# Performance work log

Measured on AMD Instinct MI355X. Metric: run time of the kernel, lower is better.

Reference implementation:

```python
import math
import jax, jax.numpy as jnp
import numpy as np

T, B, C, H = 1024, 4, 1024, 16
D = C // H  # d_k = 64


def setup_inputs() -> dict:
    key = jax.random.key(0)
    ks = jax.random.split(key, 16)
    s = 0.02
    return {
        "query": jax.random.normal(ks[0], (T, B, C), jnp.float32),
        "key": jax.random.normal(ks[1], (T, B, C), jnp.float32),
        "value": jax.random.normal(ks[2], (T, B, C), jnp.float32),
        "pos_emb": jax.random.normal(ks[3], (2 * T - 1, 1, C), jnp.float32),
        "Wq": jax.random.normal(ks[4], (C, C), jnp.float32) * s,
        "bq": jnp.zeros((C,), jnp.float32),
        "Wk": jax.random.normal(ks[5], (C, C), jnp.float32) * s,
        "bk": jnp.zeros((C,), jnp.float32),
        "Wv": jax.random.normal(ks[6], (C, C), jnp.float32) * s,
        "bv": jnp.zeros((C,), jnp.float32),
        "Wp": jax.random.normal(ks[7], (C, C), jnp.float32) * s,
        "Wo": jax.random.normal(ks[8], (C, C), jnp.float32) * s,
        "bo": jnp.zeros((C,), jnp.float32),
        "pos_bias_u": jax.random.normal(ks[9], (H, D), jnp.float32) * s,
        "pos_bias_v": jax.random.normal(ks[10], (H, D), jnp.float32) * s,
    }


def rel_shift(x):
    # x: [B, H, T, P] with P = 2T-1 -> [B, H, T, T]
    b, h, t, p = x.shape
    x = jnp.pad(x, ((0, 0), (0, 0), (0, 0), (1, 0)))  # [B,H,T,P+1]
    x = x.reshape(b, h, p + 1, t)[:, :, 1:, :].reshape(b, h, t, p)
    return x[..., : p // 2 + 1]


def reference(query, key, value, pos_emb, Wq, bq, Wk, bk, Wv, bv, Wp, Wo, bo,
              pos_bias_u, pos_bias_v):
    # T x B x C -> B x T x C
    q_in = query.transpose(1, 0, 2)
    k_in = key.transpose(1, 0, 2)
    v_in = value.transpose(1, 0, 2)
    p_in = pos_emb.transpose(1, 0, 2)  # [1, 2T-1, C]

    q = (q_in @ Wq.T + bq).reshape(B, T, H, D)            # [B,T,H,D]
    k = (k_in @ Wk.T + bk).reshape(B, T, H, D)
    v = (v_in @ Wv.T + bv).reshape(B, T, H, D)
    p = (p_in @ Wp.T).reshape(2 * T - 1, H, D)            # [2T-1,H,D]

    # content (ac) and position (bd) scores
    matrix_ac = jnp.einsum('bthd,bshd->bhts', q + pos_bias_u, k)   # [B,H,T,T]
    matrix_bd = jnp.einsum('bthd,phd->bhtp', q + pos_bias_v, p)    # [B,H,T,2T-1]
    matrix_bd = rel_shift(matrix_bd)                               # [B,H,T,T]

    scores = (matrix_ac + matrix_bd) / math.sqrt(D)
    scores = jnp.clip(scores, -1e8, 1e8)
    attn = jax.nn.softmax(scores.astype(jnp.float32), axis=-1).astype(scores.dtype)

    x = jnp.einsum('bhts,bshd->bthd', attn, v).reshape(B, T, C)
    out = x @ Wo.T + bo
    return out.transpose(1, 0, 2)  # T x B x C
```

## Files before the change

kernel.cpp:

```cpp
#include <hip/hip_runtime.h>
#include <hip/hip_bf16.h>
#include <math.h>

#define T_SEQ 1024
#define NB 4
#define NH 16
#define DD 64
#define CC 1024

typedef __attribute__((ext_vector_type(8))) short short8;
typedef __attribute__((ext_vector_type(4))) float floatx4;
typedef __attribute__((ext_vector_type(4))) unsigned short ushort4v;

#define MFMA(a, b, c) __builtin_amdgcn_mfma_f32_16x16x32_bf16((a), (b), (c), 0, 0, 0)

__device__ inline float bf2f(unsigned short u) {
  union { unsigned int i; float f; } c; c.i = ((unsigned int)u) << 16; return c.f;
}
__device__ inline unsigned short f2bf(float x) {
  union { float f; unsigned int i; } c; c.f = x;
  unsigned int u = c.i;
  u += 0x7fff + ((u >> 16) & 1);
  return (unsigned short)(u >> 16);
}

__device__ __forceinline__ void gload_lds16(const void* g, void* l) {
  __builtin_amdgcn_global_load_lds(
      (const __attribute__((address_space(1))) unsigned int*)g,
      (__attribute__((address_space(3))) unsigned int*)l, 16, 0, 0);
}

__global__ __launch_bounds__(256) void convert_kernel(
    const float* __restrict__ q, const float* __restrict__ k,
    const float* __restrict__ v, const float* __restrict__ pe_in,
    const float* __restrict__ wq, const float* __restrict__ wk,
    const float* __restrict__ wv, const float* __restrict__ wp,
    const float* __restrict__ wo,
    unsigned short* __restrict__ qo, unsigned short* __restrict__ ko,
    unsigned short* __restrict__ vo, unsigned short* __restrict__ po,
    unsigned short* __restrict__ wqo, unsigned short* __restrict__ wko,
    unsigned short* __restrict__ wvo, unsigned short* __restrict__ wpo,
    unsigned short* __restrict__ woo)
{
  const int i = blockIdx.x * 256 + threadIdx.x;
  const float* src; unsigned short* dst; int off;
  if      (i < 524288)  { src = q;     dst = qo;  off = i; }
  else if (i < 1048576) { src = k;     dst = ko;  off = i - 524288; }
  else if (i < 1572864) { src = v;     dst = vo;  off = i - 1048576; }
  else if (i < 1834880) { src = pe_in; dst = po;  off = i - 1572864; }
  else if (i < 1965952) { src = wq;    dst = wqo; off = i - 1834880; }
  else if (i < 2097024) { src = wk;    dst = wko; off = i - 1965952; }
  else if (i < 2228096) { src = wv;    dst = wvo; off = i - 2097024; }
  else if (i < 2359168) { src = wp;    dst = wpo; off = i - 2228096; }
  else if (i < 2490240) { src = wo;    dst = woo; off = i - 2359168; }
  else {
    const int j = i - 2490240;
    *(short8*)&po[2047 * 1024 + j * 8] = (short8){0, 0, 0, 0, 0, 0, 0, 0};
    return;
  }
  const float4 a0 = *(const float4*)(src + (size_t)off * 8);
  const float4 a1 = *(const float4*)(src + (size_t)off * 8 + 4);
  short8 val = (short8){(short)f2bf(a0.x), (short)f2bf(a0.y), (short)f2bf(a0.z), (short)f2bf(a0.w),
                        (short)f2bf(a1.x), (short)f2bf(a1.y), (short)f2bf(a1.z), (short)f2bf(a1.w)};
  *(short8*)&dst[(size_t)off * 8] = val;
}

template <int OUT_BF16>
__device__ __forceinline__ void gemm_core(
    const unsigned short* __restrict__ A, const unsigned short* __restrict__ Wt,
    const float* __restrict__ bias, void* __restrict__ Cv,
    unsigned short* As, unsigned short* Bs, int N, int K, int bm, int bn)
{
  const int tid = threadIdx.x;
  const int lane = tid & 63;
  const int w = tid >> 6;
  const int l15 = lane & 15, quad = lane >> 4;
  const int rw = (w >> 1) * 64, cw = (w & 1) * 64;

  floatx4 acc[4][4];
#pragma unroll
  for (int i = 0; i < 4; ++i)
#pragma unroll
    for (int j = 0; j < 4; ++j) acc[i][j] = (floatx4){0.f, 0.f, 0.f, 0.f};

  const int lrow = lane >> 2, lcol = (lane & 3) * 8;
  const unsigned short* Ag = A + (size_t)(bm + w * 32 + lrow) * K + lcol;
  const unsigned short* Wg = Wt + (size_t)(bn + w * 32 + lrow) * K + lcol;
  unsigned short* AsW = As + w * 1024;
  unsigned short* BsW = Bs + w * 1024;

  for (int k0 = 0; k0 < K; k0 += 32) {
    gload_lds16(Ag + k0, AsW);
    gload_lds16(Ag + 16 * K + k0, AsW + 512);
    gload_lds16(Wg + k0, BsW);
    gload_lds16(Wg + 16 * K + k0, BsW + 512);
    __syncthreads();

    short8 af[4], bfr[4];
#pragma unroll
    for (int i = 0; i < 4; ++i)
      af[i] = *(short8*)&As[(rw + i * 16 + l15) * 32 + quad * 8];
#pragma unroll
    for (int j = 0; j < 4; ++j)
      bfr[j] = *(short8*)&Bs[(cw + j * 16 + l15) * 32 + quad * 8];
#pragma unroll
    for (int i = 0; i < 4; ++i)
#pragma unroll
      for (int j = 0; j < 4; ++j)
        acc[i][j] = MFMA(af[i], bfr[j], acc[i][j]);
    __syncthreads();
  }

#pragma unroll
  for (int j = 0; j < 4; ++j) {
    const int col = bn + cw + j * 16 + l15;
    const float bj = bias ? bias[col] : 0.f;
#pragma unroll
    for (int i = 0; i < 4; ++i) {
      const int row0 = bm + rw + i * 16 + quad * 4;
#pragma unroll
      for (int reg = 0; reg < 4; ++reg) {
        const float v = acc[i][j][reg] + bj;
        if (OUT_BF16)
          ((unsigned short*)Cv)[(size_t)(row0 + reg) * N + col] = f2bf(v);
        else
          ((float*)Cv)[(size_t)(row0 + reg) * N + col] = v;
      }
    }
  }
}

struct GemmJob { const unsigned short* A; const unsigned short* Wt;
                 const float* bias; unsigned short* C; int mtiles; };
struct GemmJobs { GemmJob j[4]; };

__global__ __launch_bounds__(256) void gemm_qkvp(GemmJobs jobs) {
  __shared__ __align__(16) unsigned short As[128 * 32];
  __shared__ __align__(16) unsigned short Bs[128 * 32];
  GemmJob jb = jobs.j[blockIdx.z];
  if ((int)blockIdx.y >= jb.mtiles) return;
  gemm_core<1>(jb.A, jb.Wt, jb.bias, jb.C, As, Bs, 1024, 1024,
               blockIdx.y * 128, blockIdx.x * 128);
}

template <int OUT_BF16>
__global__ __launch_bounds__(256) void gemm_one(
    const unsigned short* __restrict__ A, const unsigned short* __restrict__ Wt,
    const float* __restrict__ bias, void* __restrict__ Cv) {
  __shared__ __align__(16) unsigned short As[128 * 32];
  __shared__ __align__(16) unsigned short Bs[128 * 32];
  gemm_core<OUT_BF16>(A, Wt, bias, Cv, As, Bs, 1024, 1024,
                      blockIdx.y * 128, blockIdx.x * 128);
}

__global__ __launch_bounds__(256) void transpose_v(
    const unsigned short* __restrict__ vb, unsigned short* __restrict__ vT)
{
  __shared__ __align__(16) unsigned short Lt[64 * 136];
  const int t0 = blockIdx.x * 128;
  const int h = blockIdx.y, b = blockIdx.z;
  const int tid = threadIdx.x;

#pragma unroll
  for (int cc = 0; cc < 4; ++cc) {
    const int idx = tid + cc * 256;
    const int r = idx >> 3, pc = idx & 7;
    short8 val = *(const short8*)(vb + ((size_t)((t0 + r) * 4 + b)) * 1024 + h * 64 + pc * 8);
#pragma unroll
    for (int e = 0; e < 8; ++e)
      Lt[(pc * 8 + e) * 136 + r] = (unsigned short)val[e];
  }
  __syncthreads();
#pragma unroll
  for (int cc = 0; cc < 4; ++cc) {
    const int idx = tid + cc * 256;
    const int d = idx >> 4, tc = idx & 15;
    short8 v2 = *(short8*)&Lt[d * 136 + tc * 8];
    *(short8*)(vT + ((size_t)((b * 16 + h) * 64 + d)) * 1024 + t0 + tc * 8) = v2;
  }
}

__global__ __launch_bounds__(256) void precompute_kernel(
    const unsigned short* __restrict__ kb, const unsigned short* __restrict__ pb,
    const float* __restrict__ pbu, const float* __restrict__ pbv,
    float* __restrict__ uk, float* __restrict__ vp)
{
  const int i = blockIdx.x * 256 + threadIdx.x;
  if (i < 65536) {
    const int b = i >> 14, h = (i >> 10) & 15, s = i & 1023;
    const unsigned short* kr = kb + ((size_t)(s * 4 + b)) * 1024 + h * 64;
    const float* ur = pbu + h * 64;
    float sum = 0.f;
#pragma unroll
    for (int c = 0; c < 8; ++c) {
      short8 kv = *(const short8*)(kr + c * 8);
#pragma unroll
      for (int e = 0; e < 8; ++e) sum += bf2f((unsigned short)kv[e]) * ur[c * 8 + e];
    }
    uk[i] = sum;
  } else if (i < 98304) {
    const int j = i - 65536;
    const int idx = j >> 4, h = j & 15;
    const unsigned short* pr = pb + (size_t)idx * 1024 + h * 64;
    const float* vr = pbv + h * 64;
    float sum = 0.f;
#pragma unroll
    for (int c = 0; c < 8; ++c) {
      short8 pv = *(const short8*)(pr + c * 8);
#pragma unroll
      for (int e = 0; e < 8; ++e) sum += bf2f((unsigned short)pv[e]) * vr[c * 8 + e];
    }
    vp[(idx << 4) + h] = sum;
  }
}

#define BDW 148

__global__ __launch_bounds__(256) void attn_kernel(
    const unsigned short* __restrict__ qb, const unsigned short* __restrict__ kb,
    const unsigned short* __restrict__ pb, const unsigned short* __restrict__ vT,
    const float* __restrict__ uk, const float* __restrict__ vp,
    unsigned short* __restrict__ xb)
{
  __shared__ __align__(16) float SMEM_ALL[10240];
  float* BDf  = SMEM_ALL;
  unsigned short* Pb = (unsigned short*)SMEM_ALL;
  float* uk_s  = SMEM_ALL + 9472;
  float* vp_w  = SMEM_ALL + 9600;
  float* pmax0 = SMEM_ALL + 9792;
  float* pmax1 = SMEM_ALL + 9856;
  float* psum0 = SMEM_ALL + 9920;
  float* psum1 = SMEM_ALL + 9984;
  float* m_rowA = SMEM_ALL + 10048;
  float* m_rowB = SMEM_ALL + 10112;
  float* l_row  = SMEM_ALL + 10176;

  const int tid = threadIdx.x;
  const int lane = tid & 63;
  const int w = tid >> 6;
  const int l15 = lane & 15, quad = lane >> 4;
  const int th = w & 1, sh = w >> 1;

  const int flat = blockIdx.x + (blockIdx.y << 4) + (blockIdx.z << 8);
  const int x8 = flat & 7, s8 = flat >> 3;
  const int hb = x8 * 8 + (s8 >> 4);
  const int t0 = (s8 & 15) * 64;
  const int b = hb >> 4, h = hb & 15;

  short8 qf[2][2];
#pragma unroll
  for (int tt = 0; tt < 2; ++tt)
#pragma unroll
    for (int kk = 0; kk < 2; ++kk) {
      const int t = t0 + th * 32 + tt * 16 + l15;
      qf[tt][kk] = *(const short8*)(qb + ((size_t)(t * 4 + b)) * 1024 + h * 64 + kk * 32 + quad * 8);
    }

  floatx4 of[2][2];
#pragma unroll
  for (int i = 0; i < 2; ++i)
#pragma unroll
    for (int j = 0; j < 2; ++j) of[i][j] = (floatx4){0.f, 0.f, 0.f, 0.f};

  if (tid < 64) { m_rowA[tid] = -3.0e38f; l_row[tid] = 0.f; }
  __syncthreads();

  const unsigned short* kbase = kb + ((size_t)((sh * 64 + l15) * 4 + b)) * 1024 + h * 64;
  const unsigned short* pbase0 = pb + ((size_t)(sh * 96 + l15)) * 1024 + h * 64;

  short8 kf[4][2], pf[6][2];
  {
    const int w0 = 0 - t0 + 960;
#pragma unroll
    for (int st4 = 0; st4 < 4; ++st4) {
      const unsigned short* kr = kbase + (size_t)(st4 * 16) * 4096;
      kf[st4][0] = *(const short8*)(kr + quad * 8);
      kf[st4][1] = *(const short8*)(kr + 32 + quad * 8);
    }
#pragma unroll
    for (int jt = 0; jt < 6; ++jt) {
      const int sA = sh * 96 + jt * 16 + th * 32;
      if (sA <= 16 || sA > 190) continue;
      const unsigned short* pr = pbase0 + (size_t)(w0 + jt * 16) * 1024;
      pf[jt][0] = *(const short8*)(pr + quad * 8);
      pf[jt][1] = *(const short8*)(pr + 32 + quad * 8);
    }
  }

  for (int s0 = 0; s0 < 1024; s0 += 128) {
    const int w0 = s0 - t0 + 960;
    const int par = (s0 >> 7) & 1;
    float* m_prev = par ? m_rowB : m_rowA;
    float* m_next = par ? m_rowA : m_rowB;

    if (tid < 128) uk_s[tid] = uk[((b * 16 + h) << 10) + s0 + tid];
    if (tid < 192) vp_w[tid] = vp[(((size_t)(w0 + tid)) << 4) + h];

#pragma unroll
    for (int jt = 0; jt < 6; ++jt) {
      const int jjbase = sh * 96 + jt * 16;
#pragma unroll
      for (int tt = 0; tt < 2; ++tt) {
        const int tbase = th * 32 + tt * 16;
        const int ssum = jjbase + tbase;
        if (ssum <= 32 || ssum > 190) continue;
        floatx4 z = (floatx4){0.f, 0.f, 0.f, 0.f};
        z = MFMA(pf[jt][0], qf[tt][0], z);
        z = MFMA(pf[jt][1], qf[tt][1], z);
        const int tloc = tbase + l15;
        *(float4*)&BDf[tloc * BDW + (ssum - 48) + quad * 4] =
            make_float4(z[0], z[1], z[2], z[3]);
      }
    }

    floatx4 st[4][2];
#pragma unroll
    for (int stile = 0; stile < 4; ++stile) {
#pragma unroll
      for (int tt = 0; tt < 2; ++tt) {
        floatx4 z = (floatx4){0.f, 0.f, 0.f, 0.f};
        z = MFMA(kf[stile][0], qf[tt][0], z);
        z = MFMA(kf[stile][1], qf[tt][1], z);
        st[stile][tt] = z;
      }
    }

    {
      const int s0n = (s0 + 128 < 1024) ? (s0 + 128) : 0;
      const int w0n = s0n - t0 + 960;
#pragma unroll
      for (int st4 = 0; st4 < 4; ++st4) {
        const unsigned short* kr = kbase + (size_t)(s0n + st4 * 16) * 4096;
        kf[st4][0] = *(const short8*)(kr + quad * 8);
        kf[st4][1] = *(const short8*)(kr + 32 + quad * 8);
      }
#pragma unroll
      for (int jt = 0; jt < 6; ++jt) {
        const int sA = sh * 96 + jt * 16 + th * 32;
        if (sA <= 16 || sA > 190) continue;
        const unsigned short* pr = pbase0 + (size_t)(w0n + jt * 16) * 1024;
        pf[jt][0] = *(const short8*)(pr + quad * 8);
        pf[jt][1] = *(const short8*)(pr + 32 + quad * 8);
      }
    }
    __syncthreads();

    float lmax[2] = {-3.0e38f, -3.0e38f};
#pragma unroll
    for (int stile = 0; stile < 4; ++stile)
#pragma unroll
      for (int tt = 0; tt < 2; ++tt) {
        const int tloc = th * 32 + tt * 16 + l15;
#pragma unroll
        for (int reg = 0; reg < 4; ++reg) {
          const int sloc = sh * 64 + stile * 16 + quad * 4 + reg;
          const int jj = sloc - tloc + 63;
          float v = 0.125f * (st[stile][tt][reg] + BDf[tloc * BDW + sloc - l15 + 15] +
                              uk_s[sloc] + vp_w[jj]);
          st[stile][tt][reg] = v;
          lmax[tt] = fmaxf(lmax[tt], v);
        }
      }
#pragma unroll
    for (int tt = 0; tt < 2; ++tt) {
      lmax[tt] = fmaxf(lmax[tt], __shfl_xor(lmax[tt], 16));
      lmax[tt] = fmaxf(lmax[tt], __shfl_xor(lmax[tt], 32));
    }
    if (quad == 0) {
      float* pm = sh ? pmax1 : pmax0;
      pm[th * 32 + l15] = lmax[0];
      pm[th * 32 + 16 + l15] = lmax[1];
    }
    __syncthreads();

    float mn_keep = 0.f;
    if (tid < 64) {
      const float mo = m_prev[tid];
      mn_keep = fmaxf(mo, fmaxf(pmax0[tid], pmax1[tid]));
      m_next[tid] = mn_keep;
    }
    float mt[2];
#pragma unroll
    for (int tt = 0; tt < 2; ++tt) {
      const int r = th * 32 + tt * 16 + l15;
      mt[tt] = fmaxf(m_prev[r], fmaxf(pmax0[r], pmax1[r]));
    }

    float lsum[2] = {0.f, 0.f};
#pragma unroll
    for (int stile = 0; stile < 4; ++stile)
#pragma unroll
      for (int tt = 0; tt < 2; ++tt) {
        float p0 = __expf(st[stile][tt][0] - mt[tt]);
        float p1 = __expf(st[stile][tt][1] - mt[tt]);
        float p2 = __expf(st[stile][tt][2] - mt[tt]);
        float p3 = __expf(st[stile][tt][3] - mt[tt]);
        lsum[tt] += p0 + p1 + p2 + p3;
        const int tloc = th * 32 + tt * 16 + l15;
        const int sb = sh * 64 + stile * 16 + quad * 4;
        ushort4v pk = (ushort4v){f2bf(p0), f2bf(p1), f2bf(p2), f2bf(p3)};
        *(ushort4v*)&Pb[tloc * 136 + sb] = pk;
      }
#pragma unroll
    for (int tt = 0; tt < 2; ++tt) {
      lsum[tt] += __shfl_xor(lsum[tt], 16);
      lsum[tt] += __shfl_xor(lsum[tt], 32);
    }
    if (quad == 0) {
      float* ps = sh ? psum1 : psum0;
      ps[th * 32 + l15] = lsum[0];
      ps[th * 32 + 16 + l15] = lsum[1];
    }
#pragma unroll
    for (int tt = 0; tt < 2; ++tt) {
      const int base = th * 32 + tt * 16 + quad * 4;
      const float4 mo4 = *(const float4*)&m_prev[base];
      const float4 p04 = *(const float4*)&pmax0[base];
      const float4 p14 = *(const float4*)&pmax1[base];
#pragma unroll
      for (int reg = 0; reg < 4; ++reg) {
        const float mo = ((const float*)&mo4)[reg];
        const float mn = fmaxf(mo, fmaxf(((const float*)&p04)[reg],
                                         ((const float*)&p14)[reg]));
        const float ar = __expf(mo - mn);
        of[tt][0][reg] *= ar;
        of[tt][1][reg] *= ar;
      }
    }
    __syncthreads();

    if (tid < 64) {
      const float alpha = __expf(m_prev[tid] - mn_keep);
      l_row[tid] = l_row[tid] * alpha + psum0[tid] + psum1[tid];
    }
#pragma unroll
    for (int kk2 = 0; kk2 < 4; ++kk2) {
      short8 pa[2], vf[2];
#pragma unroll
      for (int tt = 0; tt < 2; ++tt)
        pa[tt] = *(short8*)&Pb[(th * 32 + tt * 16 + l15) * 136 + kk2 * 32 + quad * 8];
#pragma unroll
      for (int dt = 0; dt < 2; ++dt)
        vf[dt] = *(const short8*)(vT + ((size_t)((b * 16 + h) * 64 + sh * 32 + dt * 16 + l15)) * 1024 +
                                  s0 + kk2 * 32 + quad * 8);
#pragma unroll
      for (int tt = 0; tt < 2; ++tt)
#pragma unroll
        for (int dt = 0; dt < 2; ++dt)
          of[tt][dt] = MFMA(pa[tt], vf[dt], of[tt][dt]);
    }
    __syncthreads();
  }

#pragma unroll
  for (int tt = 0; tt < 2; ++tt)
#pragma unroll
    for (int reg = 0; reg < 4; ++reg) {
      const int t = th * 32 + tt * 16 + quad * 4 + reg;
      const float il = 1.f / l_row[t];
#pragma unroll
      for (int dt = 0; dt < 2; ++dt) {
        const int d = sh * 32 + dt * 16 + l15;
        xb[((size_t)((t0 + t) * 4 + b)) * 1024 + h * 64 + d] = f2bf(of[tt][dt][reg] * il);
      }
    }
}

extern "C" void kernel_launch(void* const* d_in, const int* in_sizes, int n_in,
                              void* d_out, int out_size, void* d_ws, size_t ws_size,
                              hipStream_t stream) {
  const float* query   = (const float*)d_in[0];
  const float* key_    = (const float*)d_in[1];
  const float* value   = (const float*)d_in[2];
  const float* pos_emb = (const float*)d_in[3];
  const float* Wq  = (const float*)d_in[4];
  const float* bq  = (const float*)d_in[5];
  const float* Wk  = (const float*)d_in[6];
  const float* bk  = (const float*)d_in[7];
  const float* Wv  = (const float*)d_in[8];
  const float* bv  = (const float*)d_in[9];
  const float* Wp  = (const float*)d_in[10];
  const float* Wo  = (const float*)d_in[11];
  const float* bo  = (const float*)d_in[12];
  const float* pbu = (const float*)d_in[13];
  const float* pbv = (const float*)d_in[14];
  float* out = (float*)d_out;

  unsigned short* U = (unsigned short*)d_ws;
  unsigned short* qin = U;
  unsigned short* kin = U + 4194304;
  unsigned short* vin = U + 8388608;
  unsigned short* pe  = U + 12582912;
  unsigned short* wq  = U + 14680064;
  unsigned short* wk  = U + 15728640;
  unsigned short* wv  = U + 16777216;
  unsigned short* wp  = U + 17825792;
  unsigned short* wo  = U + 18874368;
  unsigned short* qb  = U + 19922944;
  unsigned short* kb  = U + 24117248;
  unsigned short* pb  = U + 28311552;
  unsigned short* vpo = U + 30408704;
  unsigned short* vTb = pe;
  unsigned short* xb  = qin;
  float* fbase = (float*)(U + 34603008);
  float* uk = fbase;
  float* vp = fbase + 65536;

  const dim3 blk(256);

  convert_kernel<<<dim3(9728), blk, 0, stream>>>(
      query, key_, value, pos_emb, Wq, Wk, Wv, Wp, Wo,
      qin, kin, vin, pe, wq, wk, wv, wp, wo);

  GemmJobs jobs;
  jobs.j[0] = GemmJob{qin, wq, bq, qb, 32};
  jobs.j[1] = GemmJob{kin, wk, bk, kb, 32};
  jobs.j[2] = GemmJob{vin, wv, bv, vpo, 32};
  jobs.j[3] = GemmJob{pe,  wp, nullptr, pb, 16};
  gemm_qkvp<<<dim3(8, 32, 4), blk, 0, stream>>>(jobs);

  transpose_v<<<dim3(8, 16, 4), blk, 0, stream>>>(vpo, vTb);

  precompute_kernel<<<dim3(384), blk, 0, stream>>>(kb, pb, pbu, pbv, uk, vp);

  attn_kernel<<<dim3(16, 16, 4), blk, 0, stream>>>(qb, kb, pb, vTb, uk, vp, xb);

  gemm_one<0><<<dim3(8, 32), blk, 0, stream>>>(xb, wo, bo, out);
}
```

Measured before the change: 343.7 us.

## Halve attention key tile to 64, shrink LDS, merge transpose and precompute kernels

The attention kernel now processes 64 keys per iteration instead of 128, shrinking the BD and P LDS buffers (about 24KB instead of 40KB) and the per-thread fragment registers, which should allow more resident workgroups per CU. __syncthreads is replaced with an explicit lgkmcnt wait plus s_barrier wrapped in sched barriers. The V transpose and the uk/vp precompute kernels are merged into a single launch to save one kernel launch. The trade-off is twice as many loop iterations, so barriers and softmax rescaling happen twice as often.

```diff
diff --git a/kernel.cpp b/kernel.cpp
--- a/kernel.cpp
+++ b/kernel.cpp
@@ -28,6 +28,13 @@
   __builtin_amdgcn_global_load_lds(
       (const __attribute__((address_space(1))) unsigned int*)g,
       (__attribute__((address_space(3))) unsigned int*)l, 16, 0, 0);
+}
+
+__device__ __forceinline__ void bar_lgkm() {
+  __builtin_amdgcn_sched_barrier(0);
+  asm volatile("s_waitcnt lgkmcnt(0)" ::: "memory");
+  __builtin_amdgcn_s_barrier();
+  __builtin_amdgcn_sched_barrier(0);
 }
 
 __global__ __launch_bounds__(256) void convert_kernel(
@@ -153,68 +160,68 @@
                       blockIdx.y * 128, blockIdx.x * 128);
 }
 
-__global__ __launch_bounds__(256) void transpose_v(
-    const unsigned short* __restrict__ vb, unsigned short* __restrict__ vT)
-{
-  __shared__ __align__(16) unsigned short Lt[64 * 136];
-  const int t0 = blockIdx.x * 128;
-  const int h = blockIdx.y, b = blockIdx.z;
-  const int tid = threadIdx.x;
-
-#pragma unroll
-  for (int cc = 0; cc < 4; ++cc) {
-    const int idx = tid + cc * 256;
-    const int r = idx >> 3, pc = idx & 7;
-    short8 val = *(const short8*)(vb + ((size_t)((t0 + r) * 4 + b)) * 1024 + h * 64 + pc * 8);
-#pragma unroll
-    for (int e = 0; e < 8; ++e)
-      Lt[(pc * 8 + e) * 136 + r] = (unsigned short)val[e];
-  }
-  __syncthreads();
-#pragma unroll
-  for (int cc = 0; cc < 4; ++cc) {
-    const int idx = tid + cc * 256;
-    const int d = idx >> 4, tc = idx & 15;
-    short8 v2 = *(short8*)&Lt[d * 136 + tc * 8];
-    *(short8*)(vT + ((size_t)((b * 16 + h) * 64 + d)) * 1024 + t0 + tc * 8) = v2;
-  }
-}
-
-__global__ __launch_bounds__(256) void precompute_kernel(
+__global__ __launch_bounds__(256) void transpose_precompute(
+    const unsigned short* __restrict__ vb, unsigned short* __restrict__ vT,
     const unsigned short* __restrict__ kb, const unsigned short* __restrict__ pb,
     const float* __restrict__ pbu, const float* __restrict__ pbv,
     float* __restrict__ uk, float* __restrict__ vp)
 {
-  const int i = blockIdx.x * 256 + threadIdx.x;
-  if (i < 65536) {
-    const int b = i >> 14, h = (i >> 10) & 15, s = i & 1023;
-    const unsigned short* kr = kb + ((size_t)(s * 4 + b)) * 1024 + h * 64;
-    const float* ur = pbu + h * 64;
-    float sum = 0.f;
-#pragma unroll
-    for (int c = 0; c < 8; ++c) {
-      short8 kv = *(const short8*)(kr + c * 8);
-#pragma unroll
-      for (int e = 0; e < 8; ++e) sum += bf2f((unsigned short)kv[e]) * ur[c * 8 + e];
-    }
-    uk[i] = sum;
-  } else if (i < 98304) {
-    const int j = i - 65536;
-    const int idx = j >> 4, h = j & 15;
-    const unsigned short* pr = pb + (size_t)idx * 1024 + h * 64;
-    const float* vr = pbv + h * 64;
-    float sum = 0.f;
-#pragma unroll
-    for (int c = 0; c < 8; ++c) {
-      short8 pv = *(const short8*)(pr + c * 8);
-#pragma unroll
-      for (int e = 0; e < 8; ++e) sum += bf2f((unsigned short)pv[e]) * vr[c * 8 + e];
-    }
-    vp[(idx << 4) + h] = sum;
+  __shared__ __align__(16) unsigned short Lt[64 * 136];
+  const int bid = blockIdx.x;
+  const int tid = threadIdx.x;
+  if (bid < 512) {
+    const int t0 = (bid & 7) * 128;
+    const int h = (bid >> 3) & 15, b = bid >> 7;
+#pragma unroll
+    for (int cc = 0; cc < 4; ++cc) {
+      const int idx = tid + cc * 256;
+      const int r = idx >> 3, pc = idx & 7;
+      short8 val = *(const short8*)(vb + ((size_t)((t0 + r) * 4 + b)) * 1024 + h * 64 + pc * 8);
+#pragma unroll
+      for (int e = 0; e < 8; ++e)
+        Lt[(pc * 8 + e) * 136 + r] = (unsigned short)val[e];
+    }
+    __syncthreads();
+#pragma unroll
+    for (int cc = 0; cc < 4; ++cc) {
+      const int idx = tid + cc * 256;
+      const int d = idx >> 4, tc = idx & 15;
+      short8 v2 = *(short8*)&Lt[d * 136 + tc * 8];
+      *(short8*)(vT + ((size_t)((b * 16 + h) * 64 + d)) * 1024 + t0 + tc * 8) = v2;
+    }
+  } else {
+    const int i = (bid - 512) * 256 + tid;
+    if (i < 65536) {
+      const int b = i >> 14, h = (i >> 10) & 15, s = i & 1023;
+      const unsigned short* kr = kb + ((size_t)(s * 4 + b)) * 1024 + h * 64;
+      const float* ur = pbu + h * 64;
+      float sum = 0.f;
+#pragma unroll
+      for (int c = 0; c < 8; ++c) {
+        short8 kv = *(const short8*)(kr + c * 8);
+#pragma unroll
+        for (int e = 0; e < 8; ++e) sum += bf2f((unsigned short)kv[e]) * ur[c * 8 + e];
+      }
+      uk[i] = sum;
+    } else if (i < 98304) {
+      const int j = i - 65536;
+      const int idx = j >> 4, h = j & 15;
+      const unsigned short* pr = pb + (size_t)idx * 1024 + h * 64;
+      const float* vr = pbv + h * 64;
+      float sum = 0.f;
+#pragma unroll
+      for (int c = 0; c < 8; ++c) {
+        short8 pv = *(const short8*)(pr + c * 8);
+#pragma unroll
+        for (int e = 0; e < 8; ++e) sum += bf2f((unsigned short)pv[e]) * vr[c * 8 + e];
+      }
+      vp[(idx << 4) + h] = sum;
+    }
   }
 }
 
-#define BDW 148
+#define BDW2 84
+#define PBW 72
 
 __global__ __launch_bounds__(256) void attn_kernel(
     const unsigned short* __restrict__ qb, const unsigned short* __restrict__ kb,
@@ -222,18 +229,18 @@
     const float* __restrict__ uk, const float* __restrict__ vp,
     unsigned short* __restrict__ xb)
 {
-  __shared__ __align__(16) float SMEM_ALL[10240];
-  float* BDf  = SMEM_ALL;
+  __shared__ __align__(16) float SMEM_ALL[6016];
+  float* BDf = SMEM_ALL;
   unsigned short* Pb = (unsigned short*)SMEM_ALL;
-  float* uk_s  = SMEM_ALL + 9472;
-  float* vp_w  = SMEM_ALL + 9600;
-  float* pmax0 = SMEM_ALL + 9792;
-  float* pmax1 = SMEM_ALL + 9856;
-  float* psum0 = SMEM_ALL + 9920;
-  float* psum1 = SMEM_ALL + 9984;
-  float* m_rowA = SMEM_ALL + 10048;
-  float* m_rowB = SMEM_ALL + 10112;
-  float* l_row  = SMEM_ALL + 10176;
+  float* uk_s  = SMEM_ALL + 5376;
+  float* vp_w  = SMEM_ALL + 5440;
+  float* pmax0 = SMEM_ALL + 5568;
+  float* pmax1 = SMEM_ALL + 5632;
+  float* psum0 = SMEM_ALL + 5696;
+  float* psum1 = SMEM_ALL + 5760;
+  float* m_rowA = SMEM_ALL + 5824;
+  float* m_rowB = SMEM_ALL + 5888;
+  float* l_row  = SMEM_ALL + 5952;
 
   const int tid = threadIdx.x;
   const int lane = tid & 63;
@@ -263,59 +270,59 @@
     for (int j = 0; j < 2; ++j) of[i][j] = (floatx4){0.f, 0.f, 0.f, 0.f};
 
   if (tid < 64) { m_rowA[tid] = -3.0e38f; l_row[tid] = 0.f; }
-  __syncthreads();
-
-  const unsigned short* kbase = kb + ((size_t)((sh * 64 + l15) * 4 + b)) * 1024 + h * 64;
-  const unsigned short* pbase0 = pb + ((size_t)(sh * 96 + l15)) * 1024 + h * 64;
-
-  short8 kf[4][2], pf[6][2];
+  bar_lgkm();
+
+  const unsigned short* kbase = kb + ((size_t)((sh * 32 + l15) * 4 + b)) * 1024 + h * 64;
+  const unsigned short* pbase0 = pb + ((size_t)(sh * 64 + l15)) * 1024 + h * 64;
+
+  short8 kf[2][2], pf[4][2];
   {
     const int w0 = 0 - t0 + 960;
 #pragma unroll
-    for (int st4 = 0; st4 < 4; ++st4) {
+    for (int st4 = 0; st4 < 2; ++st4) {
       const unsigned short* kr = kbase + (size_t)(st4 * 16) * 4096;
       kf[st4][0] = *(const short8*)(kr + quad * 8);
       kf[st4][1] = *(const short8*)(kr + 32 + quad * 8);
     }
 #pragma unroll
-    for (int jt = 0; jt < 6; ++jt) {
-      const int sA = sh * 96 + jt * 16 + th * 32;
-      if (sA <= 16 || sA > 190) continue;
+    for (int jt = 0; jt < 4; ++jt) {
+      const int sA = sh * 64 + th * 32 + jt * 16;
+      if (sA < 32 || sA > 112) continue;
       const unsigned short* pr = pbase0 + (size_t)(w0 + jt * 16) * 1024;
       pf[jt][0] = *(const short8*)(pr + quad * 8);
       pf[jt][1] = *(const short8*)(pr + 32 + quad * 8);
     }
   }
 
-  for (int s0 = 0; s0 < 1024; s0 += 128) {
+  for (int s0 = 0; s0 < 1024; s0 += 64) {
     const int w0 = s0 - t0 + 960;
-    const int par = (s0 >> 7) & 1;
+    const int par = (s0 >> 6) & 1;
     float* m_prev = par ? m_rowB : m_rowA;
     float* m_next = par ? m_rowA : m_rowB;
 
-    if (tid < 128) uk_s[tid] = uk[((b * 16 + h) << 10) + s0 + tid];
-    if (tid < 192) vp_w[tid] = vp[(((size_t)(w0 + tid)) << 4) + h];
-
-#pragma unroll
-    for (int jt = 0; jt < 6; ++jt) {
-      const int jjbase = sh * 96 + jt * 16;
+    if (tid < 64)  uk_s[tid] = uk[((b * 16 + h) << 10) + s0 + tid];
+    if (tid < 128) vp_w[tid] = vp[(((size_t)(w0 + tid)) << 4) + h];
+
+#pragma unroll
+    for (int jt = 0; jt < 4; ++jt) {
+      const int jjbase = sh * 64 + jt * 16;
 #pragma unroll
       for (int tt = 0; tt < 2; ++tt) {
         const int tbase = th * 32 + tt * 16;
         const int ssum = jjbase + tbase;
-        if (ssum <= 32 || ssum > 190) continue;
+        if (ssum <= 32 || ssum > 126) continue;
         floatx4 z = (floatx4){0.f, 0.f, 0.f, 0.f};
         z = MFMA(pf[jt][0], qf[tt][0], z);
         z = MFMA(pf[jt][1], qf[tt][1], z);
         const int tloc = tbase + l15;
-        *(float4*)&BDf[tloc * BDW + (ssum - 48) + quad * 4] =
+        *(float4*)&BDf[tloc * BDW2 + (ssum - 48) + quad * 4] =
             make_float4(z[0], z[1], z[2], z[3]);
       }
     }
 
-    floatx4 st[4][2];
-#pragma unroll
-    for (int stile = 0; stile < 4; ++stile) {
+    floatx4 st[2][2];
+#pragma unroll
+    for (int stile = 0; stile < 2; ++stile) {
 #pragma unroll
       for (int tt = 0; tt < 2; ++tt) {
         floatx4 z = (floatx4){0.f, 0.f, 0.f, 0.f};
@@ -326,36 +333,36 @@
     }
 
     {
-      const int s0n = (s0 + 128 < 1024) ? (s0 + 128) : 0;
+      const int s0n = (s0 + 64 < 1024) ? (s0 + 64) : 0;
       const int w0n = s0n - t0 + 960;
 #pragma unroll
-      for (int st4 = 0; st4 < 4; ++st4) {
+      for (int st4 = 0; st4 < 2; ++st4) {
         const unsigned short* kr = kbase + (size_t)(s0n + st4 * 16) * 4096;
         kf[st4][0] = *(const short8*)(kr + quad * 8);
         kf[st4][1] = *(const short8*)(kr + 32 + quad * 8);
       }
 #pragma unroll
-      for (int jt = 0; jt < 6; ++jt) {
-        const int sA = sh * 96 + jt * 16 + th * 32;
-        if (sA <= 16 || sA > 190) continue;
+      for (int jt = 0; jt < 4; ++jt) {
+        const int sA = sh * 64 + th * 32 + jt * 16;
+        if (sA < 32 || sA > 112) continue;
         const unsigned short* pr = pbase0 + (size_t)(w0n + jt * 16) * 1024;
         pf[jt][0] = *(const short8*)(pr + quad * 8);
         pf[jt][1] = *(const short8*)(pr + 32 + quad * 8);
       }
     }
-    __syncthreads();
+    bar_lgkm();
 
     float lmax[2] = {-3.0e38f, -3.0e38f};
 #pragma unroll
-    for (int stile = 0; stile < 4; ++stile)
+    for (int stile = 0; stile < 2; ++stile)
 #pragma unroll
       for (int tt = 0; tt < 2; ++tt) {
         const int tloc = th * 32 + tt * 16 + l15;
 #pragma unroll
         for (int reg = 0; reg < 4; ++reg) {
-          const int sloc = sh * 64 + stile * 16 + quad * 4 + reg;
+          const int sloc = sh * 32 + stile * 16 + quad * 4 + reg;
           const int jj = sloc - tloc + 63;
-          float v = 0.125f * (st[stile][tt][reg] + BDf[tloc * BDW + sloc - l15 + 15] +
+          float v = 0.125f * (st[stile][tt][reg] + BDf[tloc * BDW2 + sloc - l15 + 15] +
                               uk_s[sloc] + vp_w[jj]);
           st[stile][tt][reg] = v;
           lmax[tt] = fmaxf(lmax[tt], v);
@@ -371,7 +378,7 @@
       pm[th * 32 + l15] = lmax[0];
       pm[th * 32 + 16 + l15] = lmax[1];
     }
-    __syncthreads();
+    bar_lgkm();
 
     float mn_keep = 0.f;
     if (tid < 64) {
@@ -388,7 +395,7 @@
 
     float lsum[2] = {0.f, 0.f};
 #pragma unroll
-    for (int stile = 0; stile < 4; ++stile)
+    for (int stile = 0; stile < 2; ++stile)
 #pragma unroll
       for (int tt = 0; tt < 2; ++tt) {
         float p0 = __expf(st[stile][tt][0] - mt[tt]);
@@ -397,9 +404,9 @@
         float p3 = __expf(st[stile][tt][3] - mt[tt]);
         lsum[tt] += p0 + p1 + p2 + p3;
         const int tloc = th * 32 + tt * 16 + l15;
-        const int sb = sh * 64 + stile * 16 + quad * 4;
+        const int sb = sh * 32 + stile * 16 + quad * 4;
         ushort4v pk = (ushort4v){f2bf(p0), f2bf(p1), f2bf(p2), f2bf(p3)};
-        *(ushort4v*)&Pb[tloc * 136 + sb] = pk;
+        *(ushort4v*)&Pb[tloc * PBW + sb] = pk;
       }
 #pragma unroll
     for (int tt = 0; tt < 2; ++tt) {
@@ -427,18 +434,18 @@
         of[tt][1][reg] *= ar;
       }
     }
-    __syncthreads();
+    bar_lgkm();
 
     if (tid < 64) {
       const float alpha = __expf(m_prev[tid] - mn_keep);
       l_row[tid] = l_row[tid] * alpha + psum0[tid] + psum1[tid];
     }
 #pragma unroll
-    for (int kk2 = 0; kk2 < 4; ++kk2) {
+    for (int kk2 = 0; kk2 < 2; ++kk2) {
       short8 pa[2], vf[2];
 #pragma unroll
       for (int tt = 0; tt < 2; ++tt)
-        pa[tt] = *(short8*)&Pb[(th * 32 + tt * 16 + l15) * 136 + kk2 * 32 + quad * 8];
+        pa[tt] = *(short8*)&Pb[(th * 32 + tt * 16 + l15) * PBW + kk2 * 32 + quad * 8];
 #pragma unroll
       for (int dt = 0; dt < 2; ++dt)
         vf[dt] = *(const short8*)(vT + ((size_t)((b * 16 + h) * 64 + sh * 32 + dt * 16 + l15)) * 1024 +
@@ -449,7 +456,7 @@
         for (int dt = 0; dt < 2; ++dt)
           of[tt][dt] = MFMA(pa[tt], vf[dt], of[tt][dt]);
     }
-    __syncthreads();
+    bar_lgkm();
   }
 
 #pragma unroll
@@ -519,9 +526,8 @@
   jobs.j[3] = GemmJob{pe,  wp, nullptr, pb, 16};
   gemm_qkvp<<<dim3(8, 32, 4), blk, 0, stream>>>(jobs);
 
-  transpose_v<<<dim3(8, 16, 4), blk, 0, stream>>>(vpo, vTb);
-
-  precompute_kernel<<<dim3(384), blk, 0, stream>>>(kb, pb, pbu, pbv, uk, vp);
+  transpose_precompute<<<dim3(896), blk, 0, stream>>>(
+      vpo, vTb, kb, pb, pbu, pbv, uk, vp);
 
   attn_kernel<<<dim3(16, 16, 4), blk, 0, stream>>>(qb, kb, pb, vTb, uk, vp, xb);
 
```

Result: no change. 350.3 us (+1.9%).

## Double-buffer GEMM LDS tiles and merge transpose with precompute kernel

Applied to the files above, without the earlier changes.

The shared GEMM core now uses two LDS buffers, so the async global-to-LDS load of the next K slice is issued before the MFMAs on the current slice. This halves the barriers per K step and hides load latency, at the cost of doubling LDS per block, which may lower occupancy. Separately, the V transpose and the uk/vp precompute kernels are merged into one launch, removing one kernel launch and the gap between them.

```diff
diff --git a/kernel.cpp b/kernel.cpp
--- a/kernel.cpp
+++ b/kernel.cpp
@@ -66,10 +66,12 @@
 }
 
 template <int OUT_BF16>
-__device__ __forceinline__ void gemm_core(
+__device__ __forceinline__ void gemm_core_db(
     const unsigned short* __restrict__ A, const unsigned short* __restrict__ Wt,
     const float* __restrict__ bias, void* __restrict__ Cv,
-    unsigned short* As, unsigned short* Bs, int N, int K, int bm, int bn)
+    unsigned short* As0, unsigned short* Bs0,
+    unsigned short* As1, unsigned short* Bs1,
+    int N, int K, int bm, int bn)
 {
   const int tid = threadIdx.x;
   const int lane = tid & 63;
@@ -86,30 +88,44 @@
   const int lrow = lane >> 2, lcol = (lane & 3) * 8;
   const unsigned short* Ag = A + (size_t)(bm + w * 32 + lrow) * K + lcol;
   const unsigned short* Wg = Wt + (size_t)(bn + w * 32 + lrow) * K + lcol;
-  unsigned short* AsW = As + w * 1024;
-  unsigned short* BsW = Bs + w * 1024;
-
-  for (int k0 = 0; k0 < K; k0 += 32) {
-    gload_lds16(Ag + k0, AsW);
-    gload_lds16(Ag + 16 * K + k0, AsW + 512);
-    gload_lds16(Wg + k0, BsW);
-    gload_lds16(Wg + 16 * K + k0, BsW + 512);
-    __syncthreads();
-
-    short8 af[4], bfr[4];
-#pragma unroll
-    for (int i = 0; i < 4; ++i)
-      af[i] = *(short8*)&As[(rw + i * 16 + l15) * 32 + quad * 8];
-#pragma unroll
-    for (int j = 0; j < 4; ++j)
-      bfr[j] = *(short8*)&Bs[(cw + j * 16 + l15) * 32 + quad * 8];
-#pragma unroll
-    for (int i = 0; i < 4; ++i)
-#pragma unroll
-      for (int j = 0; j < 4; ++j)
-        acc[i][j] = MFMA(af[i], bfr[j], acc[i][j]);
+
+#define G_STAGE(AS, BS, KOFF)                                   \
+  do {                                                          \
+    gload_lds16(Ag + (KOFF), (AS) + w * 1024);                  \
+    gload_lds16(Ag + 16 * K + (KOFF), (AS) + w * 1024 + 512);   \
+    gload_lds16(Wg + (KOFF), (BS) + w * 1024);                  \
+    gload_lds16(Wg + 16 * K + (KOFF), (BS) + w * 1024 + 512);   \
+  } while (0)
+
+#define G_COMPUTE(AS, BS)                                               \
+  do {                                                                  \
+    short8 af[4], bfr[4];                                               \
+    _Pragma("unroll")                                                   \
+    for (int i = 0; i < 4; ++i)                                         \
+      af[i] = *(short8*)&(AS)[(rw + i * 16 + l15) * 32 + quad * 8];     \
+    _Pragma("unroll")                                                   \
+    for (int j = 0; j < 4; ++j)                                         \
+      bfr[j] = *(short8*)&(BS)[(cw + j * 16 + l15) * 32 + quad * 8];    \
+    _Pragma("unroll")                                                   \
+    for (int i = 0; i < 4; ++i)                                         \
+      _Pragma("unroll")                                                 \
+      for (int j = 0; j < 4; ++j)                                       \
+        acc[i][j] = MFMA(af[i], bfr[j], acc[i][j]);                     \
+  } while (0)
+
+  G_STAGE(As0, Bs0, 0);
+  __syncthreads();
+
+  for (int k0 = 0; k0 < K; k0 += 64) {
+    if (k0 + 32 < K) G_STAGE(As1, Bs1, k0 + 32);
+    G_COMPUTE(As0, Bs0);
+    __syncthreads();
+    if (k0 + 64 < K) G_STAGE(As0, Bs0, k0 + 64);
+    G_COMPUTE(As1, Bs1);
     __syncthreads();
   }
+#undef G_STAGE
+#undef G_COMPUTE
 
 #pragma unroll
   for (int j = 0; j < 4; ++j) {
@@ -135,82 +151,85 @@
 struct GemmJobs { GemmJob j[4]; };
 
 __global__ __launch_bounds__(256) void gemm_qkvp(GemmJobs jobs) {
-  __shared__ __align__(16) unsigned short As[128 * 32];
-  __shared__ __align__(16) unsigned short Bs[128 * 32];
+  __shared__ __align__(16) unsigned short As0[128 * 32];
+  __shared__ __align__(16) unsigned short Bs0[128 * 32];
+  __shared__ __align__(16) unsigned short As1[128 * 32];
+  __shared__ __align__(16) unsigned short Bs1[128 * 32];
   GemmJob jb = jobs.j[blockIdx.z];
   if ((int)blockIdx.y >= jb.mtiles) return;
-  gemm_core<1>(jb.A, jb.Wt, jb.bias, jb.C, As, Bs, 1024, 1024,
-               blockIdx.y * 128, blockIdx.x * 128);
+  gemm_core_db<1>(jb.A, jb.Wt, jb.bias, jb.C, As0, Bs0, As1, Bs1,
+                  1024, 1024, blockIdx.y * 128, blockIdx.x * 128);
 }
 
 template <int OUT_BF16>
 __global__ __launch_bounds__(256) void gemm_one(
     const unsigned short* __restrict__ A, const unsigned short* __restrict__ Wt,
     const float* __restrict__ bias, void* __restrict__ Cv) {
-  __shared__ __align__(16) unsigned short As[128 * 32];
-  __shared__ __align__(16) unsigned short Bs[128 * 32];
-  gemm_core<OUT_BF16>(A, Wt, bias, Cv, As, Bs, 1024, 1024,
-                      blockIdx.y * 128, blockIdx.x * 128);
-}
-
-__global__ __launch_bounds__(256) void transpose_v(
-    const unsigned short* __restrict__ vb, unsigned short* __restrict__ vT)
-{
-  __shared__ __align__(16) unsigned short Lt[64 * 136];
-  const int t0 = blockIdx.x * 128;
-  const int h = blockIdx.y, b = blockIdx.z;
-  const int tid = threadIdx.x;
-
-#pragma unroll
-  for (int cc = 0; cc < 4; ++cc) {
-    const int idx = tid + cc * 256;
-    const int r = idx >> 3, pc = idx & 7;
-    short8 val = *(const short8*)(vb + ((size_t)((t0 + r) * 4 + b)) * 1024 + h * 64 + pc * 8);
-#pragma unroll
-    for (int e = 0; e < 8; ++e)
-      Lt[(pc * 8 + e) * 136 + r] = (unsigned short)val[e];
-  }
-  __syncthreads();
-#pragma unroll
-  for (int cc = 0; cc < 4; ++cc) {
-    const int idx = tid + cc * 256;
-    const int d = idx >> 4, tc = idx & 15;
-    short8 v2 = *(short8*)&Lt[d * 136 + tc * 8];
-    *(short8*)(vT + ((size_t)((b * 16 + h) * 64 + d)) * 1024 + t0 + tc * 8) = v2;
-  }
-}
-
-__global__ __launch_bounds__(256) void precompute_kernel(
+  __shared__ __align__(16) unsigned short As0[128 * 32];
+  __shared__ __align__(16) unsigned short Bs0[128 * 32];
+  __shared__ __align__(16) unsigned short As1[128 * 32];
+  __shared__ __align__(16) unsigned short Bs1[128 * 32];
+  gemm_core_db<OUT_BF16>(A, Wt, bias, Cv, As0, Bs0, As1, Bs1,
+                         1024, 1024, blockIdx.y * 128, blockIdx.x * 128);
+}
+
+__global__ __launch_bounds__(256) void transpose_precompute(
+    const unsigned short* __restrict__ vb, unsigned short* __restrict__ vT,
     const unsigned short* __restrict__ kb, const unsigned short* __restrict__ pb,
     const float* __restrict__ pbu, const float* __restrict__ pbv,
     float* __restrict__ uk, float* __restrict__ vp)
 {
-  const int i = blockIdx.x * 256 + threadIdx.x;
-  if (i < 65536) {
-    const int b = i >> 14, h = (i >> 10) & 15, s = i & 1023;
-    const unsigned short* kr = kb + ((size_t)(s * 4 + b)) * 1024 + h * 64;
-    const float* ur = pbu + h * 64;
-    float sum = 0.f;
-#pragma unroll
-    for (int c = 0; c < 8; ++c) {
-      short8 kv = *(const short8*)(kr + c * 8);
-#pragma unroll
-      for (int e = 0; e < 8; ++e) sum += bf2f((unsigned short)kv[e]) * ur[c * 8 + e];
-    }
-    uk[i] = sum;
-  } else if (i < 98304) {
-    const int j = i - 65536;
-    const int idx = j >> 4, h = j & 15;
-    const unsigned short* pr = pb + (size_t)idx * 1024 + h * 64;
-    const float* vr = pbv + h * 64;
-    float sum = 0.f;
-#pragma unroll
-    for (int c = 0; c < 8; ++c) {
-      short8 pv = *(const short8*)(pr + c * 8);
-#pragma unroll
-      for (int e = 0; e < 8; ++e) sum += bf2f((unsigned short)pv[e]) * vr[c * 8 + e];
-    }
-    vp[(idx << 4) + h] = sum;
+  __shared__ __align__(16) unsigned short Lt[64 * 136];
+  const int bid = blockIdx.x;
+  const int tid = threadIdx.x;
+  if (bid < 512) {
+    const int t0 = (bid & 7) * 128;
+    const int h = (bid >> 3) & 15, b = bid >> 7;
+#pragma unroll
+    for (int cc = 0; cc < 4; ++cc) {
+      const int idx = tid + cc * 256;
+      const int r = idx >> 3, pc = idx & 7;
+      short8 val = *(const short8*)(vb + ((size_t)((t0 + r) * 4 + b)) * 1024 + h * 64 + pc * 8);
+#pragma unroll
+      for (int e = 0; e < 8; ++e)
+        Lt[(pc * 8 + e) * 136 + r] = (unsigned short)val[e];
+    }
+    __syncthreads();
+#pragma unroll
+    for (int cc = 0; cc < 4; ++cc) {
+      const int idx = tid + cc * 256;
+      const int d = idx >> 4, tc = idx & 15;
+      short8 v2 = *(short8*)&Lt[d * 136 + tc * 8];
+      *(short8*)(vT + ((size_t)((b * 16 + h) * 64 + d)) * 1024 + t0 + tc * 8) = v2;
+    }
+  } else {
+    const int i = (bid - 512) * 256 + tid;
+    if (i < 65536) {
+      const int b = i >> 14, h = (i >> 10) & 15, s = i & 1023;
+      const unsigned short* kr = kb + ((size_t)(s * 4 + b)) * 1024 + h * 64;
+      const float* ur = pbu + h * 64;
+      float sum = 0.f;
+#pragma unroll
+      for (int c = 0; c < 8; ++c) {
+        short8 kv = *(const short8*)(kr + c * 8);
+#pragma unroll
+        for (int e = 0; e < 8; ++e) sum += bf2f((unsigned short)kv[e]) * ur[c * 8 + e];
+      }
+      uk[i] = sum;
+    } else if (i < 98304) {
+      const int j = i - 65536;
+      const int idx = j >> 4, h = j & 15;
+      const unsigned short* pr = pb + (size_t)idx * 1024 + h * 64;
+      const float* vr = pbv + h * 64;
+      float sum = 0.f;
+#pragma unroll
+      for (int c = 0; c < 8; ++c) {
+        short8 pv = *(const short8*)(pr + c * 8);
+#pragma unroll
+        for (int e = 0; e < 8; ++e) sum += bf2f((unsigned short)pv[e]) * vr[c * 8 + e];
+      }
+      vp[(idx << 4) + h] = sum;
+    }
   }
 }
 
@@ -519,9 +538,8 @@
   jobs.j[3] = GemmJob{pe,  wp, nullptr, pb, 16};
   gemm_qkvp<<<dim3(8, 32, 4), blk, 0, stream>>>(jobs);
 
-  transpose_v<<<dim3(8, 16, 4), blk, 0, stream>>>(vpo, vTb);
-
-  precompute_kernel<<<dim3(384), blk, 0, stream>>>(kb, pb, pbu, pbv, uk, vp);
+  transpose_precompute<<<dim3(896), blk, 0, stream>>>(
+      vpo, vTb, kb, pb, pbu, pbv, uk, vp);
 
   attn_kernel<<<dim3(16, 16, 4), blk, 0, stream>>>(qb, kb, pb, vTb, uk, vp, xb);
 
```

After: 331.2 us. -3.6%, faster.
